# Kernel optimization log

Hardware: AMD Instinct MI355X
Metric: run time of the kernel (lower is better)

The kernel has to match this reference:

```python
import jax, jax.numpy as jnp
import numpy as np
from jax import lax

T = 8
TAU = 2.0
V_TH = 1.0
V_RESET = 0.0
ALPHA = 2.0  # ATan surrogate width


@jax.custom_vjp
def spike(x):
    # Heaviside forward, ATan surrogate backward (spikingjelly surrogate.ATan)
    return (x >= 0.0).astype(x.dtype)

def _spike_fwd(x):
    return spike(x), x

def _spike_bwd(x, g):
    pi_half_alpha = jnp.asarray(np.pi / 2.0 * ALPHA, x.dtype)
    grad = (ALPHA / 2.0) / (1.0 + (pi_half_alpha * x) ** 2)
    return (g * grad,)

spike.defvjp(_spike_fwd, _spike_bwd)


def lif_multistep(x_seq):
    # x_seq: [T, ...]; hard-reset LIF with decay_input=True:
    #   v <- v + (x - (v - v_reset)) / tau ; s = H(v - v_th) ; v <- (1-s)*v + s*v_reset
    v0 = jnp.full(x_seq.shape[1:], V_RESET, x_seq.dtype)
    def step(v, x):
        v = v + (x - (v - V_RESET)) / TAU
        s = spike(v - V_TH)
        v = (1.0 - s) * v + s * V_RESET
        return v, s
    _, s_seq = lax.scan(step, v0, x_seq)
    return s_seq


def conv2d(x, w, b, stride):
    y = lax.conv_general_dilated(x, w, (stride, stride), 'VALID',
                                 dimension_numbers=('NCHW', 'OIHW', 'NCHW'))
    return y + b[None, :, None, None]


def seq_conv(x_seq, w, b, stride):
    # SeqToANNContainer: fold T into batch, run conv, unfold
    t, bsz = x_seq.shape[0], x_seq.shape[1]
    y = conv2d(x_seq.reshape((t * bsz,) + x_seq.shape[2:]), w, b, stride)
    return y.reshape((t, bsz) + y.shape[1:])


def setup_inputs() -> dict:
    key = jax.random.key(0)
    ks = jax.random.split(key, 12)
    s = 0.05
    return {
        'x':    jax.random.normal(ks[0], (512, 4, 84, 84), jnp.float32),
        'w1':   jax.random.normal(ks[1], (32, 4, 8, 8), jnp.float32) * s,
        'b1':   jax.random.normal(ks[2], (32,), jnp.float32) * s,
        'w2':   jax.random.normal(ks[3], (64, 32, 4, 4), jnp.float32) * s,
        'b2':   jax.random.normal(ks[4], (64,), jnp.float32) * s,
        'w3':   jax.random.normal(ks[5], (64, 64, 3, 3), jnp.float32) * s,
        'b3':   jax.random.normal(ks[6], (64,), jnp.float32) * s,
        'fw1':  jax.random.normal(ks[7], (512, 64 * 7 * 7), jnp.float32) * s,
        'fb1':  jax.random.normal(ks[8], (512,), jnp.float32) * s,
        'fw2':  jax.random.normal(ks[9], (6, 512), jnp.float32) * s,
        'fb2':  jax.random.normal(ks[10], (6,), jnp.float32) * s,
    }


def reference(x, w1, b1, w2, b2, w3, b3, fw1, fb1, fw2, fb2):
    # static conv, then replicate across T timesteps
    h = conv2d(x, w1, b1, 4)                      # [B,32,20,20]
    x_seq = jnp.broadcast_to(h[None], (T,) + h.shape)
    s = lif_multistep(x_seq)                      # [T,B,32,20,20]
    s = lif_multistep(seq_conv(s, w2, b2, 2))     # [T,B,64,9,9]
    s = lif_multistep(seq_conv(s, w3, b3, 1))     # [T,B,64,7,7]
    flat = s.reshape(T, s.shape[1], -1)           # [T,B,3136]
    s = lif_multistep(jnp.einsum('tbi,oi->tbo', flat, fw1) + fb1)  # [T,B,512]
    out = s.mean(axis=0)                          # [B,512]
    return out @ fw2.T + fb2                      # [B,6]
```

## Files before the change

### kernel.cpp

```cpp
#include <hip/hip_runtime.h>
#include <cstdint>

#define RFL(x) __builtin_amdgcn_readfirstlane(x)

static constexpr int B  = 512;
static constexpr int C0 = 4,  H0 = 84, W0 = 84;
static constexpr int C1 = 32, H1 = 20, W1 = 20, P1 = H1 * W1;
static constexpr int C2 = 64, H2 = 9,  W2 = 9,  P2 = H2 * W2;
static constexpr int C3 = 64, H3 = 7,  W3 = 7,  P3 = H3 * W3;
static constexpr int K  = C3 * P3;
static constexpr int O  = 512;
static constexpr int NJOB2 = B * P2;

static constexpr size_t OFF_S1   = 0;
static constexpr size_t OFF_S2   = 6553600;
static constexpr size_t OFF_S3   = OFF_S2 + 2654208;
static constexpr size_t OFF_W2T  = OFF_S3 + 1605632;
static constexpr size_t OFF_W3T  = OFF_W2T + 131072 + 256;
static constexpr size_t OFF_FW1T = OFF_W3T + 147456;
static constexpr size_t OFF_W1T  = OFF_FW1T + 6422528;
static constexpr size_t OFF_CNT  = OFF_W1T + 32768;
static constexpr size_t OFF_EVT  = OFF_CNT + (size_t)NJOB2 * 32;
static constexpr size_t WS_NEEDED = OFF_EVT + (size_t)NJOB2 * 1152;

__global__ void k_prep_all(const float* __restrict__ w1, float* __restrict__ w1T,
                           const float* __restrict__ w2, float* __restrict__ w2T,
                           const float* __restrict__ w3, float* __restrict__ w3T) {
    int n = blockIdx.x * 256 + threadIdx.x;
    if (n < 8192) {
        int kx = n & 7, o = (n >> 3) & 7, ky = (n >> 6) & 7, ic = (n >> 9) & 3, o8 = n >> 11;
        int oc = o8 * 8 + o;
        w1T[n] = w1[((oc * 4 + ic) * 8 + ky) * 8 + kx];
        return;
    }
    n -= 8192;
    if (n < 32768 + 64) {
        if (n >= 32768) { w2T[n] = 0.0f; return; }
        int oc = n >> 9, r = n & 511;
        int ic = r >> 4, ky = (r >> 2) & 3, kx = r & 3;
        w2T[((ky * 4 + kx) * 32 + ic) * 64 + oc] = w2[n];
        return;
    }
    n -= 32768 + 64;
    if (n < 36864) {
        int oc = n / 576, r = n - oc * 576;
        int ic = r / 9, rr = r - ic * 9;
        int ky = rr / 3, kx = rr - ky * 3;
        w3T[((ky * 3 + kx) * 64 + ic) * 64 + oc] = w3[n];
    }
}

__global__ __launch_bounds__(256) void k_prep_fw1(const float* __restrict__ fw1,
                                                  float* __restrict__ fw1T) {
    __shared__ float tile[64][65];
    int ot = blockIdx.x & 7;
    int it = blockIdx.x >> 3;
    int tr = threadIdx.x >> 6;
    int tc = threadIdx.x & 63;
    #pragma unroll
    for (int r = 0; r < 16; r++) {
        int ol = r * 4 + tr;
        tile[ol][tc] = fw1[(size_t)(ot * 64 + ol) * K + it * 64 + tc];
    }
    __syncthreads();
    #pragma unroll
    for (int r = 0; r < 16; r++) {
        int il = r * 4 + tr;
        fw1T[(size_t)(it * 64 + il) * O + ot * 64 + tc] = tile[tc][il];
    }
}

__global__ __launch_bounds__(256) void k_conv1(const float* __restrict__ x,
                                               const float* __restrict__ w1T,
                                               const float* __restrict__ b1,
                                               uint8_t* __restrict__ s1c) {
    int blk = blockIdx.x;
    int o8  = blk / 400;
    int rest = (blk - o8 * 400) * 256 + threadIdx.x;
    int img = rest / 200, pair = rest - img * 200;
    int oy  = pair / 10;
    int ox0 = (pair - oy * 10) * 2;
    const float* xb = x + (size_t)img * 28224 + (size_t)(oy * 4) * W0 + ox0 * 4;
    const float* wh = w1T + o8 * 2048;

    float acc[2][8];
    #pragma unroll
    for (int pp = 0; pp < 2; pp++)
        #pragma unroll
        for (int o = 0; o < 8; o++) acc[pp][o] = b1[o8 * 8 + o];

    #pragma unroll 1
    for (int ic = 0; ic < C0; ic++) {
        #pragma unroll 1
        for (int ky = 0; ky < 8; ky++) {
            const float* rp = xb + ic * 7056 + ky * W0;
            float4 a0 = *(const float4*)rp;
            float4 a1 = *(const float4*)(rp + 4);
            float4 a2 = *(const float4*)(rp + 8);
            float xv[12] = {a0.x, a0.y, a0.z, a0.w, a1.x, a1.y, a1.z, a1.w,
                            a2.x, a2.y, a2.z, a2.w};
            const float* wb = wh + (ic * 8 + ky) * 64;
            #pragma unroll
            for (int o = 0; o < 8; o++) {
                #pragma unroll
                for (int pp = 0; pp < 2; pp++) {
                    float s = acc[pp][o];
                    #pragma unroll
                    for (int kx = 0; kx < 8; kx++)
                        s = fmaf(wb[o * 8 + kx], xv[pp * 4 + kx], s);
                    acc[pp][o] = s;
                }
            }
        }
    }

    #pragma unroll
    for (int pp = 0; pp < 2; pp++) {
        uint32_t byc[8] = {0, 0, 0, 0, 0, 0, 0, 0};
        #pragma unroll
        for (int o = 0; o < 8; o++) {
            float h = acc[pp][o], v = 0.f;
            uint32_t mm = 0;
            #pragma unroll
            for (int t = 0; t < 8; t++) {
                v = v + (h - v) * 0.5f;
                bool sp = (v >= 1.0f);
                mm |= sp ? (1u << t) : 0u;
                v = sp ? 0.f : v;
            }
            uint32_t fs = mm & (0u - mm);
            #pragma unroll
            for (int c = 0; c < 8; c++) byc[c] |= ((fs >> c) & 1u) << o;
        }
        int pix = oy * W1 + ox0 + pp;
        uint8_t* op = s1c + (size_t)(img * P1 + pix) * 32 + o8;
        #pragma unroll
        for (int c = 0; c < 8; c++) op[c * 4] = (uint8_t)byc[c];
    }
}

__global__ __launch_bounds__(256) void k_evt(const uint8_t* __restrict__ s1c,
                                             uint32_t* __restrict__ cnt,
                                             uint16_t* __restrict__ evl) {
    __shared__ __align__(16) uint16_t buf[32][576];
    int tid = threadIdx.x;
    int jl  = tid >> 3;
    int job = blockIdx.x * 32 + jl;
    int c   = tid & 7;
    int b = job / P2, pix = job - b * P2;
    int oy = pix / W2, ox = pix - oy * W2;
    const uint8_t* sb = s1c + (size_t)b * P1 * 32 + c * 4;

    int count = 0;
    #pragma unroll
    for (int pos = 0; pos < 16; pos++) {
        int ipix = (oy * 2 + (pos >> 2)) * W1 + ox * 2 + (pos & 3);
        count += __popc(*(const uint32_t*)(sb + (size_t)ipix * 32));
    }
    int padded = (count + 7) & ~7;

    int incl = padded;
    #pragma unroll
    for (int d = 1; d < 8; d <<= 1) {
        int t = __shfl_up(incl, d, 8);
        if ((tid & 7) >= d) incl += t;
    }
    uint16_t* out = &buf[jl][incl - padded];

    int k = 0;
    #pragma unroll 1
    for (int pos = 0; pos < 16; pos++) {
        int ipix = (oy * 2 + (pos >> 2)) * W1 + ox * 2 + (pos & 3);
        uint32_t w = *(const uint32_t*)(sb + (size_t)ipix * 32);
        while (w) {
            int i = __builtin_ctz(w);
            w &= w - 1;
            out[k++] = (uint16_t)((pos << 5) + i);
        }
    }
    while (k < padded) out[k++] = 512;
    cnt[job * 8 + c] = (uint32_t)padded;

    __syncthreads();
    const uint4* src = (const uint4*)&buf[0][0];
    uint4* dst = (uint4*)(evl + (size_t)blockIdx.x * 32 * 576);
    #pragma unroll
    for (int i = 0; i < 9; i++) dst[tid + i * 256] = src[tid + i * 256];
}

__global__ __launch_bounds__(256) void k_conv2_ev(const uint32_t* __restrict__ cnt,
                                                  const uint16_t* __restrict__ evl,
                                                  const float* __restrict__ w2T,
                                                  const float* __restrict__ b2,
                                                  uint8_t* __restrict__ s2p) {
    int wid = RFL(blockIdx.x * 4 + (threadIdx.x >> 6));
    int lane = threadIdx.x & 63;
    int b = wid / P2, pix = wid - b * P2;
    const uint32_t* evw = (const uint32_t*)(evl + (size_t)wid * 576);
    const uint32_t* cp  = cnt + wid * 8;
    float A[8];
    #pragma unroll
    for (int c = 0; c < 8; c++) A[c] = 0.f;
    int kw = 0;
    #define CLS(c)                                                            \
    {   int n = (int)cp[c];                                                   \
        for (int k = 0; k < n; k += 8) {                                      \
            uint32_t d0 = evw[kw], d1 = evw[kw + 1];                          \
            uint32_t d2 = evw[kw + 2], d3 = evw[kw + 3]; kw += 4;             \
            float v0 = w2T[(d0 & 0xffffu) * 64 + lane];                       \
            float v1 = w2T[(d0 >> 16)    * 64 + lane];                        \
            float v2 = w2T[(d1 & 0xffffu) * 64 + lane];                       \
            float v3 = w2T[(d1 >> 16)    * 64 + lane];                        \
            float v4 = w2T[(d2 & 0xffffu) * 64 + lane];                       \
            float v5 = w2T[(d2 >> 16)    * 64 + lane];                        \
            float v6 = w2T[(d3 & 0xffffu) * 64 + lane];                       \
            float v7 = w2T[(d3 >> 16)    * 64 + lane];                        \
            A[c] += v0; A[c] += v1; A[c] += v2; A[c] += v3;                   \
            A[c] += v4; A[c] += v5; A[c] += v6; A[c] += v7;                   \
        }                                                                     \
    }
    CLS(0) CLS(1) CLS(2) CLS(3) CLS(4) CLS(5) CLS(6) CLS(7)
    #undef CLS

    float y[8];
    y[0] = A[0];
    y[1] = A[0] + A[1];
    y[2] = A[0] + A[2];
    y[3] = A[0] + A[1] + A[3];
    y[4] = A[0] + A[4];
    y[5] = A[0] + A[1] + A[2] + A[5];
    y[6] = A[0] + A[6];
    y[7] = A[0] + A[1] + A[3] + A[7];

    float bo = b2[lane];
    uint32_t mout = 0;
    float v = 0.f;
    #pragma unroll
    for (int t = 0; t < 8; t++) {
        float yt = y[t] + bo;
        v = v + (yt - v) * 0.5f;
        bool sp = (v >= 1.0f);
        mout |= sp ? (1u << t) : 0u;
        v = sp ? 0.f : v;
    }
    unsigned long long* op = (unsigned long long*)(s2p + (size_t)(b * P2 + pix) * 64);
    #pragma unroll
    for (int t = 0; t < 8; t++) {
        unsigned long long bm = __ballot((mout >> t) & 1u);
        if (lane == 0) op[t] = bm;
    }
}

__global__ __launch_bounds__(256) void k_conv2_old(const uint8_t* __restrict__ s1c,
                                                   const float* __restrict__ w2T,
                                                   const float* __restrict__ b2,
                                                   uint8_t* __restrict__ s2p) {
    int wid = blockIdx.x * 4 + (threadIdx.x >> 6);
    int lane = threadIdx.x & 63;
    int b = wid / P2, pix = wid - b * P2;
    int oy = pix / W2, ox = pix - oy * W2;
    float A[8];
    #pragma unroll
    for (int c = 0; c < 8; c++) A[c] = 0.f;
    #pragma unroll
    for (int ky = 0; ky < 4; ky++) {
        #pragma unroll
        for (int kx = 0; kx < 4; kx++) {
            int mofs = RFL((b * P1 + (oy * 2 + ky) * W1 + (ox * 2 + kx)) * 32);
            const uint32_t* mp = (const uint32_t*)(s1c + mofs);
            const float* wp = w2T + (ky * 4 + kx) * 32 * 64 + lane;
            uint32_t w0 = mp[0], w1 = mp[1], w2 = mp[2], w3 = mp[3];
            uint32_t w4 = mp[4], w5 = mp[5], w6 = mp[6], w7 = mp[7];
            while (w0 | w1 | w2 | w3 | w4 | w5 | w6 | w7) {
                if (w0) { int i = __builtin_ctz(w0); w0 &= w0 - 1; A[0] += wp[i * 64]; }
                if (w1) { int i = __builtin_ctz(w1); w1 &= w1 - 1; A[1] += wp[i * 64]; }
                if (w2) { int i = __builtin_ctz(w2); w2 &= w2 - 1; A[2] += wp[i * 64]; }
                if (w3) { int i = __builtin_ctz(w3); w3 &= w3 - 1; A[3] += wp[i * 64]; }
                if (w4) { int i = __builtin_ctz(w4); w4 &= w4 - 1; A[4] += wp[i * 64]; }
                if (w5) { int i = __builtin_ctz(w5); w5 &= w5 - 1; A[5] += wp[i * 64]; }
                if (w6) { int i = __builtin_ctz(w6); w6 &= w6 - 1; A[6] += wp[i * 64]; }
                if (w7) { int i = __builtin_ctz(w7); w7 &= w7 - 1; A[7] += wp[i * 64]; }
            }
        }
    }
    float y[8];
    y[0] = A[0];
    y[1] = A[0] + A[1];
    y[2] = A[0] + A[2];
    y[3] = A[0] + A[1] + A[3];
    y[4] = A[0] + A[4];
    y[5] = A[0] + A[1] + A[2] + A[5];
    y[6] = A[0] + A[6];
    y[7] = A[0] + A[1] + A[3] + A[7];
    float bo = b2[lane];
    uint32_t mout = 0;
    float v = 0.f;
    #pragma unroll
    for (int t = 0; t < 8; t++) {
        float yt = y[t] + bo;
        v = v + (yt - v) * 0.5f;
        bool sp = (v >= 1.0f);
        mout |= sp ? (1u << t) : 0u;
        v = sp ? 0.f : v;
    }
    unsigned long long* op = (unsigned long long*)(s2p + (size_t)(b * P2 + pix) * 64);
    #pragma unroll
    for (int t = 0; t < 8; t++) {
        unsigned long long bm = __ballot((mout >> t) & 1u);
        if (lane == 0) op[t] = bm;
    }
}

__global__ __launch_bounds__(256) void k_conv3(const uint8_t* __restrict__ s2p,
                                               const float* __restrict__ w3T,
                                               const float* __restrict__ b3,
                                               uint8_t* __restrict__ s3m) {
    int wid = blockIdx.x * 4 + (threadIdx.x >> 6);
    int lane = threadIdx.x & 63;
    int b = wid / P3, pix = wid - b * P3;
    int oy = pix / W3, ox = pix - oy * W3;
    float A[8];
    #pragma unroll
    for (int t = 0; t < 8; t++) A[t] = 0.f;
    #pragma unroll
    for (int ky = 0; ky < 3; ky++) {
        #pragma unroll
        for (int kx = 0; kx < 3; kx++) {
            int mofs = RFL((b * P2 + (oy + ky) * W2 + (ox + kx)) * 64);
            const unsigned long long* mp = (const unsigned long long*)(s2p + mofs);
            const float* wp = w3T + (ky * 3 + kx) * 64 * 64 + lane;
            unsigned long long m0 = mp[0], m1 = mp[1], m2 = mp[2], m3 = mp[3];
            unsigned long long m4 = mp[4], m5 = mp[5], m6 = mp[6], m7 = mp[7];
            while (m0 | m1 | m2 | m3 | m4 | m5 | m6 | m7) {
                if (m0) { int i = __builtin_ctzll(m0); m0 &= m0 - 1; A[0] += wp[i * 64]; }
                if (m1) { int i = __builtin_ctzll(m1); m1 &= m1 - 1; A[1] += wp[i * 64]; }
                if (m2) { int i = __builtin_ctzll(m2); m2 &= m2 - 1; A[2] += wp[i * 64]; }
                if (m3) { int i = __builtin_ctzll(m3); m3 &= m3 - 1; A[3] += wp[i * 64]; }
                if (m4) { int i = __builtin_ctzll(m4); m4 &= m4 - 1; A[4] += wp[i * 64]; }
                if (m5) { int i = __builtin_ctzll(m5); m5 &= m5 - 1; A[5] += wp[i * 64]; }
                if (m6) { int i = __builtin_ctzll(m6); m6 &= m6 - 1; A[6] += wp[i * 64]; }
                if (m7) { int i = __builtin_ctzll(m7); m7 &= m7 - 1; A[7] += wp[i * 64]; }
            }
        }
    }
    float bo = b3[lane];
    uint32_t mout = 0;
    float v = 0.f;
    #pragma unroll
    for (int t = 0; t < 8; t++) {
        float y = A[t] + bo;
        v = v + (y - v) * 0.5f;
        bool sp = (v >= 1.0f);
        mout |= sp ? (1u << t) : 0u;
        v = sp ? 0.f : v;
    }
    s3m[(size_t)(b * P3 + pix) * 64 + lane] = (uint8_t)mout;
}

__global__ __launch_bounds__(256) void k_fc(const uint8_t* __restrict__ s3m,
                                            const float* __restrict__ fw1T,
                                            const float* __restrict__ fb1,
                                            const float* __restrict__ fw2,
                                            const float* __restrict__ fb2,
                                            float* __restrict__ out) {
    __shared__ float red[3][64][65];
    int b = blockIdx.x;
    int w = threadIdx.x >> 6;
    int lane = threadIdx.x & 63;
    float acc[8][8];
    #pragma unroll
    for (int j = 0; j < 8; j++)
        #pragma unroll
        for (int t = 0; t < 8; t++) acc[j][t] = 0.f;

    int ibeg = w * 784;
    for (int i0 = ibeg; i0 < ibeg + 784; i0 += 16) {
        int base = RFL(b * K + i0);
        const uint32_t* mp = (const uint32_t*)(s3m + base);
        #pragma unroll
        for (int d = 0; d < 4; d++) {
            uint32_t md = mp[d];
            if (md == 0) continue;
            #pragma unroll
            for (int q = 0; q < 4; q++) {
                uint32_t m = (md >> (q * 8)) & 0xffu;
                if (m == 0) continue;
                int i_our = i0 + d * 4 + q;
                int pix = i_our >> 6, c = i_our & 63;
                const float4* wp = (const float4*)(fw1T + (size_t)(c * 49 + pix) * O + lane * 8);
                float4 wa = wp[0], wb = wp[1];
                float wv[8] = {wa.x, wa.y, wa.z, wa.w, wb.x, wb.y, wb.z, wb.w};
                #pragma unroll
                for (int t = 0; t < 8; t++) {
                    if (m & (1u << t)) {
                        #pragma unroll
                        for (int j = 0; j < 8; j++) acc[j][t] += wv[j];
                    }
                }
            }
        }
    }

    if (w > 0) {
        #pragma unroll
        for (int j = 0; j < 8; j++)
            #pragma unroll
            for (int t = 0; t < 8; t++) red[w - 1][lane][j * 8 + t] = acc[j][t];
    }
    __syncthreads();
    if (w != 0) return;

    #pragma unroll
    for (int ww = 0; ww < 3; ww++)
        #pragma unroll
        for (int j = 0; j < 8; j++)
            #pragma unroll
            for (int t = 0; t < 8; t++) acc[j][t] += red[ww][lane][j * 8 + t];

    float msum[8];
    #pragma unroll
    for (int j = 0; j < 8; j++) {
        float yb = fb1[lane * 8 + j];
        float v = 0.f, cntt = 0.f;
        #pragma unroll
        for (int t = 0; t < 8; t++) {
            float y = acc[j][t] + yb;
            v = v + (y - v) * 0.5f;
            bool sp = (v >= 1.0f);
            cntt += sp ? 1.f : 0.f;
            v = sp ? 0.f : v;
        }
        msum[j] = cntt * 0.125f;
    }
    #pragma unroll
    for (int kk = 0; kk < 6; kk++) {
        const float* wr = fw2 + kk * O + lane * 8;
        float pv = 0.f;
        #pragma unroll
        for (int j = 0; j < 8; j++) pv += msum[j] * wr[j];
        #pragma unroll
        for (int off = 32; off > 0; off >>= 1) pv += __shfl_down(pv, off, 64);
        if (lane == 0) out[b * 6 + kk] = pv + fb2[kk];
    }
}

extern "C" void kernel_launch(void* const* d_in, const int* in_sizes, int n_in,
                              void* d_out, int out_size, void* d_ws, size_t ws_size,
                              hipStream_t stream) {
    const float* x   = (const float*)d_in[0];
    const float* w1  = (const float*)d_in[1];
    const float* b1  = (const float*)d_in[2];
    const float* w2  = (const float*)d_in[3];
    const float* b2  = (const float*)d_in[4];
    const float* w3  = (const float*)d_in[5];
    const float* b3  = (const float*)d_in[6];
    const float* fw1 = (const float*)d_in[7];
    const float* fb1 = (const float*)d_in[8];
    const float* fw2 = (const float*)d_in[9];
    const float* fb2 = (const float*)d_in[10];
    float* out = (float*)d_out;

    uint8_t*  ws   = (uint8_t*)d_ws;
    uint8_t*  s1c  = ws + OFF_S1;
    uint8_t*  s2p  = ws + OFF_S2;
    uint8_t*  s3m  = ws + OFF_S3;
    float*    w2T  = (float*)(ws + OFF_W2T);
    float*    w3T  = (float*)(ws + OFF_W3T);
    float*    fw1T = (float*)(ws + OFF_FW1T);
    float*    w1T  = (float*)(ws + OFF_W1T);
    uint32_t* cnt  = (uint32_t*)(ws + OFF_CNT);
    uint16_t* evl  = (uint16_t*)(ws + OFF_EVT);

    hipLaunchKernelGGL(k_prep_all, dim3(305),   dim3(256), 0, stream,
                       w1, w1T, w2, w2T, w3, w3T);
    hipLaunchKernelGGL(k_prep_fw1, dim3(392),   dim3(256), 0, stream, fw1, fw1T);
    hipLaunchKernelGGL(k_conv1,    dim3(1600),  dim3(256), 0, stream, x, w1T, b1, s1c);
    if (ws_size >= WS_NEEDED) {
        hipLaunchKernelGGL(k_evt,      dim3(1296),  dim3(256), 0, stream, s1c, cnt, evl);
        hipLaunchKernelGGL(k_conv2_ev, dim3(10368), dim3(256), 0, stream, cnt, evl, w2T, b2, s2p);
    } else {
        hipLaunchKernelGGL(k_conv2_old, dim3(10368), dim3(256), 0, stream, s1c, w2T, b2, s2p);
    }
    hipLaunchKernelGGL(k_conv3,    dim3(6272),  dim3(256), 0, stream, s2p, w3T, b3, s3m);
    hipLaunchKernelGGL(k_fc,       dim3(512),   dim3(256), 0, stream, s3m, fw1T, fb1, fw2, fb2, out);
}
```

Measured before the change: 168.8 us.

## Split conv1 input channels across two half-blocks with shared-memory reduction

Each block now handles 128 output-pixel pairs, and its two halves each cover two of the four input channels. The partial sums are combined through shared memory before the LIF epilogue. Block order is also changed so the four o8 groups for the same pixels run in adjacent blocks, which should improve L2 reuse of the input. This doubles the grid and the per-thread parallelism at the cost of a shared-memory reduction, a barrier, and half the threads sitting idle in the epilogue.

```diff
diff --git a/kernel.cpp b/kernel.cpp
--- a/kernel.cpp
+++ b/kernel.cpp
@@ -74,45 +74,61 @@
                                                const float* __restrict__ w1T,
                                                const float* __restrict__ b1,
                                                uint8_t* __restrict__ s1c) {
+    __shared__ float red[128][16];
     int blk = blockIdx.x;
-    int o8  = blk / 400;
-    int rest = (blk - o8 * 400) * 256 + threadIdx.x;
-    int img = rest / 200, pair = rest - img * 200;
+    int o8  = blk & 3;
+    int grp = blk >> 2;
+    int tid = threadIdx.x;
+    int ih  = tid >> 7;
+    int jl  = tid & 127;
+    int job = grp * 128 + jl;
+    int img = job / 200, pair = job - img * 200;
     int oy  = pair / 10;
     int ox0 = (pair - oy * 10) * 2;
-    const float* xb = x + (size_t)img * 28224 + (size_t)(oy * 4) * W0 + ox0 * 4;
-    const float* wh = w1T + o8 * 2048;
+    const float* xb = x + (size_t)img * 28224 + (size_t)(ih * 2) * 7056
+                        + (size_t)(oy * 4) * W0 + ox0 * 4;
+    const float* wh = w1T + o8 * 2048 + ih * 1024;
 
     float acc[2][8];
     #pragma unroll
     for (int pp = 0; pp < 2; pp++)
         #pragma unroll
-        for (int o = 0; o < 8; o++) acc[pp][o] = b1[o8 * 8 + o];
+        for (int o = 0; o < 8; o++) acc[pp][o] = ih ? 0.f : b1[o8 * 8 + o];
 
     #pragma unroll 1
-    for (int ic = 0; ic < C0; ic++) {
-        #pragma unroll 1
-        for (int ky = 0; ky < 8; ky++) {
-            const float* rp = xb + ic * 7056 + ky * W0;
-            float4 a0 = *(const float4*)rp;
-            float4 a1 = *(const float4*)(rp + 4);
-            float4 a2 = *(const float4*)(rp + 8);
-            float xv[12] = {a0.x, a0.y, a0.z, a0.w, a1.x, a1.y, a1.z, a1.w,
-                            a2.x, a2.y, a2.z, a2.w};
-            const float* wb = wh + (ic * 8 + ky) * 64;
-            #pragma unroll
-            for (int o = 0; o < 8; o++) {
+    for (int it = 0; it < 16; it++) {
+        const float* rp = xb + (it >> 3) * 7056 + (it & 7) * W0;
+        float4 a0 = *(const float4*)rp;
+        float4 a1 = *(const float4*)(rp + 4);
+        float4 a2 = *(const float4*)(rp + 8);
+        float xv[12] = {a0.x, a0.y, a0.z, a0.w, a1.x, a1.y, a1.z, a1.w,
+                        a2.x, a2.y, a2.z, a2.w};
+        const float* wb = wh + (it >> 3) * 512 + (it & 7) * 64;
+        #pragma unroll
+        for (int o = 0; o < 8; o++) {
+            #pragma unroll
+            for (int pp = 0; pp < 2; pp++) {
+                float s = acc[pp][o];
                 #pragma unroll
-                for (int pp = 0; pp < 2; pp++) {
-                    float s = acc[pp][o];
-                    #pragma unroll
-                    for (int kx = 0; kx < 8; kx++)
-                        s = fmaf(wb[o * 8 + kx], xv[pp * 4 + kx], s);
-                    acc[pp][o] = s;
-                }
+                for (int kx = 0; kx < 8; kx++)
+                    s = fmaf(wb[o * 8 + kx], xv[pp * 4 + kx], s);
+                acc[pp][o] = s;
             }
         }
     }
+
+    if (ih) {
+        #pragma unroll
+        for (int pp = 0; pp < 2; pp++)
+            #pragma unroll
+            for (int o = 0; o < 8; o++) red[jl][pp * 8 + o] = acc[pp][o];
+    }
+    __syncthreads();
+    if (ih) return;
+    #pragma unroll
+    for (int pp = 0; pp < 2; pp++)
+        #pragma unroll
+        for (int o = 0; o < 8; o++) acc[pp][o] += red[jl][pp * 8 + o];
 
     #pragma unroll
     for (int pp = 0; pp < 2; pp++) {
@@ -474,7 +490,7 @@
     hipLaunchKernelGGL(k_prep_all, dim3(305),   dim3(256), 0, stream,
                        w1, w1T, w2, w2T, w3, w3T);
     hipLaunchKernelGGL(k_prep_fw1, dim3(392),   dim3(256), 0, stream, fw1, fw1T);
-    hipLaunchKernelGGL(k_conv1,    dim3(1600),  dim3(256), 0, stream, x, w1T, b1, s1c);
+    hipLaunchKernelGGL(k_conv1,    dim3(3200),  dim3(256), 0, stream, x, w1T, b1, s1c);
     if (ws_size >= WS_NEEDED) {
         hipLaunchKernelGGL(k_evt,      dim3(1296),  dim3(256), 0, stream, s1c, cnt, evl);
         hipLaunchKernelGGL(k_conv2_ev, dim3(10368), dim3(256), 0, stream, cnt, evl, w2T, b2, s2p);
```

After: 239.3 us. +41.8%, slower.
